# Performance work log

Hardware: AMD Instinct MI355X
Metric: run time of the kernel (lower is better)

The kernel has to match this reference:

```python
import jax, jax.numpy as jnp
import numpy as np

H, EXP, N, CONV = 1024, 2, 16, 4
INNER = H * EXP          # 2048
DTR = max(H // 16, 1)    # 64
BATCH, SEQ = 2, 1024


def setup_inputs() -> dict:
    key = jax.random.key(0)
    ks = jax.random.split(key, 16)
    g = lambda k, shape, s=0.02: (jax.random.normal(k, shape, dtype=jnp.float32) * s)
    return {
        "x": jax.random.normal(ks[0], (BATCH, SEQ, H), dtype=jnp.float32),
        "norm_w": jnp.ones((H,), jnp.float32),
        "norm_b": jnp.zeros((H,), jnp.float32),
        "in_w": g(ks[1], (H, 2 * INNER)),
        "in_b": jnp.zeros((2 * INNER,), jnp.float32),
        "conv_w": g(ks[2], (INNER, CONV), 0.1),   # depthwise kernel (torch weight[:,0,:])
        "conv_b": jnp.zeros((INNER,), jnp.float32),
        "bc_w": g(ks[3], (INNER, 2 * N)),
        "bc_b": jnp.zeros((2 * N,), jnp.float32),
        "dtr_w": g(ks[4], (INNER, DTR)),
        "dtr_b": jnp.zeros((DTR,), jnp.float32),
        "dt_w": g(ks[5], (DTR, INNER)),
        "dt_b": jnp.zeros((INNER,), jnp.float32),
        "out_w": g(ks[6], (INNER, H)),
        "out_b": jnp.zeros((H,), jnp.float32),
    }


def _forward(x, norm_w, norm_b, in_w, in_b, conv_w, conv_b,
             bc_w, bc_b, dtr_w, dtr_b, dt_w, dt_b, out_w, out_b):
    B, L, _ = x.shape
    # LayerNorm
    mu = x.mean(-1, keepdims=True)
    var = ((x - mu) ** 2).mean(-1, keepdims=True)
    normed = (x - mu) * jax.lax.rsqrt(var + 1e-5) * norm_w + norm_b
    # in_proj -> split x/z branches
    xz = normed @ in_w + in_b
    xb, z = xz[..., :INNER], xz[..., INNER:]
    # causal depthwise conv (torch pads both sides conv-1 then truncates to L == left-pad only)
    xp = jnp.pad(xb, ((0, 0), (CONV - 1, 0), (0, 0)))
    xc = sum(xp[:, k:k + L, :] * conv_w[:, k] for k in range(CONV)) + conv_b
    xa = jax.nn.silu(xc)                                  # [B,L,INNER]
    # B, C, dt projections
    bc = xa @ bc_w + bc_b
    Bm, Cm = bc[..., :N], bc[..., N:]                     # each [B,L,N]
    dt = jax.nn.softplus((xa @ dtr_w + dtr_b) @ dt_w + dt_b)
    dt = jnp.clip(dt, 0.001, 0.1)                         # [B,L,INNER]
    # discretize
    a_diag = -(jnp.arange(N, dtype=jnp.float32) + 1.0)
    a_bar = jnp.exp(dt[..., None] * a_diag)               # [B,L,INNER,N]
    dt_mean = dt.mean(axis=2, keepdims=True)[..., None]   # [B,L,1,1]
    bx = dt_mean * Bm[:, :, None, :] * xa[..., None]      # [B,L,INNER,N]
    # selective scan over time (h = a_t*h + bx_t; y_t = <C_t, h_t>)
    def step(h, ts):
        a_t, bx_t, c_t = ts
        h = a_t * h + bx_t
        y = jnp.einsum('bdn,bn->bd', h, c_t)
        return h, y
    h0 = jnp.zeros((B, INNER, N), x.dtype)
    _, ys = jax.lax.scan(step, h0, (a_bar.transpose(1, 0, 2, 3),
                                    bx.transpose(1, 0, 2, 3),
                                    Cm.transpose(1, 0, 2)))
    ssm_out = ys.transpose(1, 0, 2)                       # [B,L,INNER]
    gated = ssm_out * jax.nn.silu(z)
    return gated @ out_w + out_b


def reference(x, norm_w, norm_b, in_w, in_b, conv_w, conv_b,
              bc_w, bc_b, dtr_w, dtr_b, dt_w, dt_b, out_w, out_b):
    return _forward(x, norm_w, norm_b, in_w, in_b, conv_w, conv_b,
                    bc_w, bc_b, dtr_w, dtr_b, dt_w, dt_b, out_w, out_b)
```

## Files before the change

kernel.cpp:

```cpp
#include <hip/hip_runtime.h>
#include <math.h>

#define H      1024
#define INNER  2048
#define NST    16
#define SEQ    1024
#define ROWS   2048
#define XZW    (2*INNER)

typedef unsigned short u16;
typedef short bf16x8 __attribute__((ext_vector_type(8)));
typedef float f32x4 __attribute__((ext_vector_type(4)));

__device__ __forceinline__ u16 f2bf(float f) {
  unsigned u = __float_as_uint(f);
  return (u16)((u + 0x7FFF + ((u >> 16) & 1)) >> 16);
}
__device__ __forceinline__ float bf2f(u16 s) {
  return __uint_as_float(((unsigned)s) << 16);
}
__device__ __forceinline__ void gload16(const u16* g, u16* l) {
  __builtin_amdgcn_global_load_lds(
      (const __attribute__((address_space(1))) void*)g,
      (__attribute__((address_space(3))) void*)l, 16, 0, 0);
}

__global__ __launch_bounds__(256) void ln_kernel(
    const float* __restrict__ x, const float* __restrict__ w,
    const float* __restrict__ b, u16* __restrict__ ahi, u16* __restrict__ alo) {
  int row = blockIdx.x;
  int tid = threadIdx.x;
  const float4* xr = reinterpret_cast<const float4*>(x + (size_t)row * H);
  float4 v = xr[tid];
  float s = v.x + v.y + v.z + v.w;
  for (int o = 32; o > 0; o >>= 1) s += __shfl_down(s, o);
  __shared__ float r1[4], r2[4];
  int wv = tid >> 6;
  if ((tid & 63) == 0) r1[wv] = s;
  __syncthreads();
  float mu = (r1[0] + r1[1] + r1[2] + r1[3]) * (1.0f / H);
  float4 d;
  d.x = v.x - mu; d.y = v.y - mu; d.z = v.z - mu; d.w = v.w - mu;
  float sq = d.x*d.x + d.y*d.y + d.z*d.z + d.w*d.w;
  for (int o = 32; o > 0; o >>= 1) sq += __shfl_down(sq, o);
  if ((tid & 63) == 0) r2[wv] = sq;
  __syncthreads();
  float var = (r2[0] + r2[1] + r2[2] + r2[3]) * (1.0f / H);
  float rs = 1.0f / sqrtf(var + 1e-5f);
  float4 w4 = reinterpret_cast<const float4*>(w)[tid];
  float4 b4 = reinterpret_cast<const float4*>(b)[tid];
  float o0 = d.x * rs * w4.x + b4.x;
  float o1 = d.y * rs * w4.y + b4.y;
  float o2 = d.z * rs * w4.z + b4.z;
  float o3 = d.w * rs * w4.w + b4.w;
  ushort4 hh, ll;
  hh.x = f2bf(o0); ll.x = f2bf(o0 - bf2f(hh.x));
  hh.y = f2bf(o1); ll.y = f2bf(o1 - bf2f(hh.y));
  hh.z = f2bf(o2); ll.z = f2bf(o2 - bf2f(hh.z));
  hh.w = f2bf(o3); ll.w = f2bf(o3 - bf2f(hh.w));
  reinterpret_cast<ushort4*>(ahi + (size_t)row * H)[tid] = hh;
  reinterpret_cast<ushort4*>(alo + (size_t)row * H)[tid] = ll;
}

__global__ __launch_bounds__(256) void cvt_t_kernel(
    const float* __restrict__ W, u16* __restrict__ Thi, u16* __restrict__ Tlo,
    int K, int N) {
  __shared__ float t[32][33];
  int tx = threadIdx.x & 31, ty = threadIdx.x >> 5;
  int k0 = blockIdx.y * 32, n0 = blockIdx.x * 32;
#pragma unroll
  for (int r = 0; r < 4; ++r)
    t[ty + r * 8][tx] = W[(size_t)(k0 + ty + r * 8) * N + n0 + tx];
  __syncthreads();
#pragma unroll
  for (int r = 0; r < 4; ++r) {
    int row = ty + r * 8;
    float v = t[tx][row];
    u16 h = f2bf(v);
    size_t idx = (size_t)(n0 + row) * K + k0 + tx;
    Thi[idx] = h;
    Tlo[idx] = f2bf(v - bf2f(h));
  }
}

template <int BN_, bool ATOMIC>
__global__ __launch_bounds__(256) void gemm_mfma(
    const u16* __restrict__ a_hi, const u16* __restrict__ a_lo,
    const u16* __restrict__ b_hi, const u16* __restrict__ b_lo,
    const float* __restrict__ bias, float* __restrict__ C, int N,
    int Kstride, int Ksub) {
  constexpr int MN = BN_ / 32;
  constexpr int NB = BN_ / 16;
  constexpr int T  = 16 + 2 * NB;
  constexpr int CH = T / 4;
  constexpr int HALF = 128 * 32 * 2 + BN_ * 32 * 2;
  __shared__ __align__(16) u16 lds[2 * HALF];
  const int tid = threadIdx.x;
  const int lane = tid & 63;
  const int w = tid >> 6;
  const int m0 = blockIdx.y * 128;
  const int n0 = blockIdx.x * BN_;
  const int koff = blockIdx.z * Ksub;
  const int wr = (w >> 1) * 64;
  const int wc = (w & 1) * (BN_ / 2);
  const int s = lane >> 4;
  const int rl = lane & 15;
  f32x4 acc[4][MN];
#pragma unroll
  for (int m = 0; m < 4; ++m)
#pragma unroll
    for (int n = 0; n < MN; ++n)
#pragma unroll
      for (int r = 0; r < 4; ++r) acc[m][n][r] = 0.0f;

  auto stageF = [&](int buf, int k0) {
    u16* lbase = lds + buf * HALF;
    for (int c = w; c < T; c += 4) {
      const u16* gb; int cc, rg, lo;
      if (c < 8)            { gb = a_hi; cc = c;           rg = m0; lo = 0; }
      else if (c < 16)      { gb = a_lo; cc = c - 8;       rg = m0; lo = 128 * 32; }
      else if (c < 16 + NB) { gb = b_hi; cc = c - 16;      rg = n0; lo = 128 * 64; }
      else                  { gb = b_lo; cc = c - 16 - NB; rg = n0; lo = 128 * 64 + BN_ * 32; }
      int o = cc * 1024 + lane * 16;
      int row = o >> 6;
      int k8 = ((o >> 4) & 3) ^ ((row >> 1) & 3);
      gload16(gb + (size_t)(rg + row) * Kstride + k0 + k8 * 8,
              lbase + lo + cc * 512);
    }
  };

  const int NT = Ksub / 32;
  stageF(0, koff);
  asm volatile("s_waitcnt vmcnt(0)\n\ts_barrier" ::: "memory");
  int cur = 0;
  for (int t = 0; t < NT; ++t) {
    if (t + 1 < NT) {
      stageF(cur ^ 1, koff + (t + 1) * 32);
      if constexpr (CH == 8)
        asm volatile("s_waitcnt vmcnt(8)\n\ts_barrier" ::: "memory");
      else if constexpr (CH == 7)
        asm volatile("s_waitcnt vmcnt(7)\n\ts_barrier" ::: "memory");
      else
        asm volatile("s_waitcnt vmcnt(6)\n\ts_barrier" ::: "memory");
    } else {
      asm volatile("s_waitcnt vmcnt(0)\n\ts_barrier" ::: "memory");
    }
    const u16* lah = lds + cur * HALF;
    const u16* lal = lah + 128 * 32;
    const u16* lbh = lah + 128 * 64;
    const u16* lbl = lbh + BN_ * 32;
    bf16x8 ah[4], al[4], bh[MN], bl[MN];
#pragma unroll
    for (int m = 0; m < 4; ++m) {
      int r = wr + m * 16 + rl;
      int sw = (s ^ ((r >> 1) & 3)) * 8;
      ah[m] = *reinterpret_cast<const bf16x8*>(lah + r * 32 + sw);
      al[m] = *reinterpret_cast<const bf16x8*>(lal + r * 32 + sw);
    }
#pragma unroll
    for (int n = 0; n < MN; ++n) {
      int r = wc + n * 16 + rl;
      int sw = (s ^ ((r >> 1) & 3)) * 8;
      bh[n] = *reinterpret_cast<const bf16x8*>(lbh + r * 32 + sw);
      bl[n] = *reinterpret_cast<const bf16x8*>(lbl + r * 32 + sw);
    }
#pragma unroll
    for (int m = 0; m < 4; ++m)
#pragma unroll
      for (int n = 0; n < MN; ++n) {
        acc[m][n] = __builtin_amdgcn_mfma_f32_16x16x32_bf16(ah[m], bh[n], acc[m][n], 0, 0, 0);
        acc[m][n] = __builtin_amdgcn_mfma_f32_16x16x32_bf16(al[m], bh[n], acc[m][n], 0, 0, 0);
        acc[m][n] = __builtin_amdgcn_mfma_f32_16x16x32_bf16(ah[m], bl[n], acc[m][n], 0, 0, 0);
      }
    asm volatile("s_barrier" ::: "memory");
    cur ^= 1;
  }
#pragma unroll
  for (int n = 0; n < MN; ++n) {
    int col = n0 + wc + n * 16 + rl;
    float bv = ATOMIC ? 0.0f : bias[col];
#pragma unroll
    for (int m = 0; m < 4; ++m) {
      int r0 = m0 + wr + m * 16 + s * 4;
#pragma unroll
      for (int r = 0; r < 4; ++r) {
        if (ATOMIC)
          atomicAdd(&C[(size_t)(r0 + r) * N + col], acc[m][n][r]);
        else
          C[(size_t)(r0 + r) * N + col] = acc[m][n][r] + bv;
      }
    }
  }
}

__global__ __launch_bounds__(256) void conv_kernel(
    const float* __restrict__ xz, const float* __restrict__ cw,
    const float* __restrict__ cb, float* __restrict__ xa,
    u16* __restrict__ xahi, u16* __restrict__ xalo) {
  int row = blockIdx.x;
  int t = row & (SEQ - 1);
  int tid = threadIdx.x;
  for (int d = tid; d < INNER; d += 256) {
    float4 w = reinterpret_cast<const float4*>(cw)[d];
    float wj[4] = {w.x, w.y, w.z, w.w};
    float acc = cb[d];
#pragma unroll
    for (int j = 0; j < 4; ++j) {
      int ts = t - 3 + j;
      if (ts >= 0) acc = fmaf(xz[(size_t)(row - 3 + j) * XZW + d], wj[j], acc);
    }
    float sv = acc / (1.0f + __expf(-acc));
    size_t idx = (size_t)row * INNER + d;
    xa[idx] = sv;
    u16 hh = f2bf(sv);
    xahi[idx] = hh;
    xalo[idx] = f2bf(sv - bf2f(hh));
  }
}

__global__ __launch_bounds__(256) void bcd_init_kernel(
    const float* __restrict__ bc_b, const float* __restrict__ dtr_b,
    float* __restrict__ bcd) {
  int i = blockIdx.x * 256 + threadIdx.x;
  int col = i % 96;
  bcd[i] = (col < 32) ? bc_b[col] : dtr_b[col - 32];
}

__global__ __launch_bounds__(256) void out_init_kernel(
    const float* __restrict__ out_b, float* __restrict__ out) {
  int i = blockIdx.x * 256 + threadIdx.x;
  out[i] = out_b[i & (H - 1)];
}

__global__ __launch_bounds__(256) void dtsp_kernel(
    const float* __restrict__ bcd, const float* __restrict__ dt_w,
    const float* __restrict__ dt_b, float* __restrict__ dt,
    float* __restrict__ dtm, float* __restrict__ scanBC) {
  int tid = threadIdx.x;
  int row0 = blockIdx.x * 8;
  __shared__ float rl[8][64];
  __shared__ float psum[8][4];
  __shared__ float dtmrow[8];
  for (int i = tid; i < 512; i += 256)
    rl[i >> 6][i & 63] = bcd[(size_t)(row0 + (i >> 6)) * 96 + 32 + (i & 63)];
  __syncthreads();
  float lsum[8] = {};
  for (int j = 0; j < 8; ++j) {
    int d = tid + j * 256;
    float acc[8];
    float bb = dt_b[d];
#pragma unroll
    for (int r = 0; r < 8; ++r) acc[r] = bb;
#pragma unroll 8
    for (int k = 0; k < 64; ++k) {
      float w = dt_w[(size_t)k * INNER + d];
#pragma unroll
      for (int r = 0; r < 8; ++r) acc[r] = fmaf(rl[r][k], w, acc[r]);
    }
#pragma unroll
    for (int r = 0; r < 8; ++r) {
      float xv = acc[r];
      float sp = (xv > 15.0f) ? xv : log1pf(__expf(xv));
      float dv = fminf(fmaxf(sp, 1e-3f), 0.1f);
      dt[(size_t)(row0 + r) * INNER + d] = dv;
      lsum[r] += dv;
    }
  }
#pragma unroll
  for (int r = 0; r < 8; ++r) {
    float s = lsum[r];
    for (int o = 32; o > 0; o >>= 1) s += __shfl_down(s, o);
    if ((tid & 63) == 0) psum[r][tid >> 6] = s;
  }
  __syncthreads();
  if (tid < 8) {
    float v =
        (psum[tid][0] + psum[tid][1] + psum[tid][2] + psum[tid][3]) * (1.0f / INNER);
    dtm[row0 + tid] = v;
    dtmrow[tid] = v;
  }
  __syncthreads();
  int rr = tid >> 5, cc = tid & 31;
  float v = bcd[(size_t)(row0 + rr) * 96 + cc];
  if (cc < 16) v *= dtmrow[rr];
  scanBC[(size_t)(row0 + rr) * 32 + cc] = v;
}

__global__ __launch_bounds__(256) void scan1_kernel(
    const float* __restrict__ dt, const float* __restrict__ xa,
    const float* __restrict__ scanBC, float* __restrict__ Abuf,
    float* __restrict__ hbuf, int NC, int CL) {
  int tid = threadIdx.x;
  int dl = tid & 63;
  int NCB = NC >> 2;
  int bi = blockIdx.x;
  int cg = bi % NCB;
  int dg = (bi / NCB) & 31;
  int b = bi / (NCB * 32);
  int d = dg * 64 + dl;
  int c = cg * 4 + (tid >> 6);
  size_t r = (size_t)b * SEQ + (size_t)c * CL;
  const float* dtp = dt + r * INNER + d;
  const float* xap = xa + r * INNER + d;
  const float* bcp = scanBC + r * 32;
  float h[16];
#pragma unroll
  for (int n = 0; n < 16; ++n) h[n] = 0.0f;
  float S = 0.0f;
#pragma unroll 2
  for (int t = 0; t < CL; ++t) {
    float dtv = dtp[0];
    float xav = xap[0];
    float bB[16];
#pragma unroll
    for (int q = 0; q < 4; ++q)
      *reinterpret_cast<float4*>(&bB[q * 4]) =
          *reinterpret_cast<const float4*>(bcp + q * 4);
    S += dtv;
    float e1 = __expf(-dtv);
    float w = e1;
#pragma unroll
    for (int n = 0; n < 16; ++n) {
      h[n] = fmaf(w, h[n], xav * bB[n]);
      w *= e1;
    }
    dtp += INNER;
    xap += INNER;
    bcp += 32;
  }
  size_t base = (((size_t)b * NC + c) * INNER + d) * 16;
  float eS = __expf(-S);
  float A[16];
  float w = eS;
#pragma unroll
  for (int n = 0; n < 16; ++n) { A[n] = w; w *= eS; }
#pragma unroll
  for (int q = 0; q < 4; ++q) {
    *reinterpret_cast<float4*>(Abuf + base + q * 4) =
        *reinterpret_cast<float4*>(&A[q * 4]);
    *reinterpret_cast<float4*>(hbuf + base + q * 4) =
        *reinterpret_cast<float4*>(&h[q * 4]);
  }
}

__global__ __launch_bounds__(256) void scan2_kernel(
    const float* __restrict__ Abuf, float* __restrict__ hbuf, int NC) {
  int idx = blockIdx.x * 256 + threadIdx.x;
  size_t stride = (size_t)INNER * 16;
  size_t base = (size_t)(idx >> 15) * NC * stride + (size_t)(idx & 32767);
  float h = 0.0f;
  for (int c = 0; c < NC; ++c) {
    float A = Abuf[base];
    float hl = hbuf[base];
    hbuf[base] = h;
    h = fmaf(A, h, hl);
    base += stride;
  }
}

__global__ __launch_bounds__(256) void scan3_kernel(
    const float* __restrict__ dt, const float* __restrict__ xa,
    const float* __restrict__ scanBC, const float* __restrict__ xz,
    const float* __restrict__ hbuf, u16* __restrict__ ghi, u16* __restrict__ glo,
    int NC, int CL) {
  int tid = threadIdx.x;
  int dl = tid & 63;
  int NCB = NC >> 2;
  int bi = blockIdx.x;
  int cg = bi % NCB;
  int dg = (bi / NCB) & 31;
  int b = bi / (NCB * 32);
  int d = dg * 64 + dl;
  int c = cg * 4 + (tid >> 6);
  size_t r = (size_t)b * SEQ + (size_t)c * CL;
  const float* dtp = dt + r * INNER + d;
  const float* xap = xa + r * INNER + d;
  const float* bcp = scanBC + r * 32;
  const float* zp = xz + r * XZW + INNER + d;
  u16* ghp = ghi + r * INNER + d;
  u16* glp = glo + r * INNER + d;
  size_t hb = (((size_t)b * NC + c) * INNER + d) * 16;
  float h[16];
#pragma unroll
  for (int q = 0; q < 4; ++q)
    *reinterpret_cast<float4*>(&h[q * 4]) =
        *reinterpret_cast<const float4*>(hbuf + hb + q * 4);
#pragma unroll 2
  for (int t = 0; t < CL; ++t) {
    float dtv = dtp[0];
    float xav = xap[0];
    float zv = zp[0];
    float bB[16], cC[16];
#pragma unroll
    for (int q = 0; q < 4; ++q) {
      *reinterpret_cast<float4*>(&bB[q * 4]) =
          *reinterpret_cast<const float4*>(bcp + q * 4);
      *reinterpret_cast<float4*>(&cC[q * 4]) =
          *reinterpret_cast<const float4*>(bcp + 16 + q * 4);
    }
    float e1 = __expf(-dtv);
    float w = e1;
    float y = 0.0f;
#pragma unroll
    for (int n = 0; n < 16; ++n) {
      h[n] = fmaf(w, h[n], xav * bB[n]);
      w *= e1;
      y = fmaf(h[n], cC[n], y);
    }
    float sz = zv / (1.0f + __expf(-zv));
    float g = y * sz;
    u16 gh = f2bf(g);
    ghp[0] = gh;
    glp[0] = f2bf(g - bf2f(gh));
    dtp += INNER;
    xap += INNER;
    bcp += 32;
    zp += XZW;
    ghp += INNER;
    glp += INNER;
  }
}

extern "C" void kernel_launch(void* const* d_in, const int* in_sizes, int n_in,
                              void* d_out, int out_size, void* d_ws, size_t ws_size,
                              hipStream_t stream) {
  const float* x      = (const float*)d_in[0];
  const float* norm_w = (const float*)d_in[1];
  const float* norm_b = (const float*)d_in[2];
  const float* in_w   = (const float*)d_in[3];
  const float* in_b   = (const float*)d_in[4];
  const float* conv_w = (const float*)d_in[5];
  const float* conv_b = (const float*)d_in[6];
  const float* bc_w   = (const float*)d_in[7];
  const float* bc_b   = (const float*)d_in[8];
  const float* dtr_w  = (const float*)d_in[9];
  const float* dtr_b  = (const float*)d_in[10];
  const float* dt_w   = (const float*)d_in[11];
  const float* dt_b   = (const float*)d_in[12];
  const float* out_w  = (const float*)d_in[13];
  const float* out_b  = (const float*)d_in[14];

  float* ws = (float*)d_ws;
  float* xz     = ws;
  float* xa     = ws + 8388608;
  float* bcd    = ws + 12582912;
  float* dt     = ws + 12779520;
  float* dtm    = ws + 16973824;
  float* scanBC = ws + 16975872;
  u16* a1hi   = (u16*)(ws + 17041408);
  u16* a1lo   = (u16*)(ws + 18089984);
  u16* b1thi  = (u16*)(ws + 19138560);
  u16* b1tlo  = (u16*)(ws + 21235712);
  u16* xahi   = (u16*)(ws + 17041408);
  u16* xalo   = (u16*)(ws + 19138560);
  u16* bcdThi = (u16*)(ws + 21235712);
  u16* bcdTlo = (u16*)(ws + 21334016);
  u16* g3hi   = (u16*)(ws + 17041408);
  u16* g3lo   = (u16*)(ws + 19138560);
  u16* b3thi  = (u16*)(ws + 21235712);
  u16* b3tlo  = (u16*)(ws + 22284288);
  float* Abuf = ws + 23332864;
  const int NC = 64, CL = SEQ / NC;
  float* hbuf = Abuf + (size_t)NC * 65536;

  ln_kernel<<<ROWS, 256, 0, stream>>>(x, norm_w, norm_b, a1hi, a1lo);
  cvt_t_kernel<<<dim3(XZW / 32, H / 32), 256, 0, stream>>>(in_w, b1thi, b1tlo, H, XZW);
  gemm_mfma<128, false><<<dim3(XZW / 128, ROWS / 128, 1), 256, 0, stream>>>(
      a1hi, a1lo, b1thi, b1tlo, in_b, xz, XZW, H, H);
  conv_kernel<<<ROWS, 256, 0, stream>>>(xz, conv_w, conv_b, xa, xahi, xalo);
  cvt_t_kernel<<<dim3(1, INNER / 32), 256, 0, stream>>>(bc_w, bcdThi, bcdTlo,
                                                        INNER, 32);
  cvt_t_kernel<<<dim3(2, INNER / 32), 256, 0, stream>>>(
      dtr_w, bcdThi + 32 * 2048, bcdTlo + 32 * 2048, INNER, 64);
  bcd_init_kernel<<<ROWS * 96 / 256, 256, 0, stream>>>(bc_b, dtr_b, bcd);
  gemm_mfma<96, true><<<dim3(1, ROWS / 128, 16), 256, 0, stream>>>(
      xahi, xalo, bcdThi, bcdTlo, bc_b, bcd, 96, INNER, INNER / 16);
  dtsp_kernel<<<ROWS / 8, 256, 0, stream>>>(bcd, dt_w, dt_b, dt, dtm, scanBC);
  cvt_t_kernel<<<dim3(H / 32, INNER / 32), 256, 0, stream>>>(out_w, b3thi, b3tlo,
                                                             INNER, H);
  scan1_kernel<<<2 * 32 * (NC / 4), 256, 0, stream>>>(dt, xa, scanBC, Abuf, hbuf,
                                                      NC, CL);
  scan2_kernel<<<256, 256, 0, stream>>>(Abuf, hbuf, NC);
  scan3_kernel<<<2 * 32 * (NC / 4), 256, 0, stream>>>(dt, xa, scanBC, xz, hbuf,
                                                      g3hi, g3lo, NC, CL);
  out_init_kernel<<<ROWS * H / 256, 256, 0, stream>>>(out_b, (float*)d_out);
  gemm_mfma<64, true><<<dim3(H / 64, ROWS / 128, 2), 256, 0, stream>>>(
      g3hi, g3lo, b3thi, b3tlo, out_b, (float*)d_out, H, INNER, INNER / 2);
}
```

Before: 392.9 us.

## Replace atomic split-K accumulation with partial buffers and reduction kernels

The split-K GEMMs now write per-slice partial results into scratch buffers instead of doing fp32 atomicAdd into a pre-initialized output. Separate reduction kernels then sum the slices and add the bias. The output projection goes from 2 to 4 K-splits. This removes atomic contention and the init kernels, and the result becomes deterministic. The cost is extra scratch traffic, one more pass over memory, and reuse of the xz and Abuf buffers as scratch space.

```diff
diff --git a/kernel.cpp b/kernel.cpp
--- a/kernel.cpp
+++ b/kernel.cpp
@@ -83,12 +83,12 @@
   }
 }
 
-template <int BN_, bool ATOMIC>
+template <int BN_, int MODE>
 __global__ __launch_bounds__(256) void gemm_mfma(
     const u16* __restrict__ a_hi, const u16* __restrict__ a_lo,
     const u16* __restrict__ b_hi, const u16* __restrict__ b_lo,
     const float* __restrict__ bias, float* __restrict__ C, int N,
-    int Kstride, int Ksub) {
+    int Kstride, int Ksub, int Mtot) {
   constexpr int MN = BN_ / 32;
   constexpr int NB = BN_ / 16;
   constexpr int T  = 16 + 2 * NB;
@@ -175,22 +175,47 @@
     asm volatile("s_barrier" ::: "memory");
     cur ^= 1;
   }
+  float* Cz = (MODE == 1) ? C + (size_t)blockIdx.z * Mtot * N : C;
 #pragma unroll
   for (int n = 0; n < MN; ++n) {
     int col = n0 + wc + n * 16 + rl;
-    float bv = ATOMIC ? 0.0f : bias[col];
+    float bv = (MODE == 0) ? bias[col] : 0.0f;
 #pragma unroll
     for (int m = 0; m < 4; ++m) {
       int r0 = m0 + wr + m * 16 + s * 4;
 #pragma unroll
-      for (int r = 0; r < 4; ++r) {
-        if (ATOMIC)
-          atomicAdd(&C[(size_t)(r0 + r) * N + col], acc[m][n][r]);
-        else
-          C[(size_t)(r0 + r) * N + col] = acc[m][n][r] + bv;
-      }
-    }
-  }
+      for (int r = 0; r < 4; ++r)
+        Cz[(size_t)(r0 + r) * N + col] = acc[m][n][r] + bv;
+    }
+  }
+}
+
+__global__ __launch_bounds__(256) void red3_kernel(
+    const float* __restrict__ p, const float* __restrict__ out_b,
+    float* __restrict__ out) {
+  int i = (blockIdx.x * 256 + threadIdx.x) * 4;
+  float4 a = *reinterpret_cast<const float4*>(p + i);
+  float4 b = *reinterpret_cast<const float4*>(p + 2097152 + i);
+  float4 c = *reinterpret_cast<const float4*>(p + 2 * 2097152 + i);
+  float4 d = *reinterpret_cast<const float4*>(p + 3 * 2097152 + i);
+  float4 bb = *reinterpret_cast<const float4*>(out_b + (i & (H - 1)));
+  float4 o;
+  o.x = a.x + b.x + c.x + d.x + bb.x;
+  o.y = a.y + b.y + c.y + d.y + bb.y;
+  o.z = a.z + b.z + c.z + d.z + bb.z;
+  o.w = a.w + b.w + c.w + d.w + bb.w;
+  *reinterpret_cast<float4*>(out + i) = o;
+}
+
+__global__ __launch_bounds__(256) void redb_kernel(
+    const float* __restrict__ p, const float* __restrict__ bc_b,
+    const float* __restrict__ dtr_b, float* __restrict__ bcd) {
+  int i = blockIdx.x * 256 + threadIdx.x;
+  int col = i % 96;
+  float s = (col < 32) ? bc_b[col] : dtr_b[col - 32];
+#pragma unroll
+  for (int k = 0; k < 16; ++k) s += p[(size_t)k * (ROWS * 96) + i];
+  bcd[i] = s;
 }
 
 __global__ __launch_bounds__(256) void conv_kernel(
@@ -216,20 +241,6 @@
     xahi[idx] = hh;
     xalo[idx] = f2bf(sv - bf2f(hh));
   }
-}
-
-__global__ __launch_bounds__(256) void bcd_init_kernel(
-    const float* __restrict__ bc_b, const float* __restrict__ dtr_b,
-    float* __restrict__ bcd) {
-  int i = blockIdx.x * 256 + threadIdx.x;
-  int col = i % 96;
-  bcd[i] = (col < 32) ? bc_b[col] : dtr_b[col - 32];
-}
-
-__global__ __launch_bounds__(256) void out_init_kernel(
-    const float* __restrict__ out_b, float* __restrict__ out) {
-  int i = blockIdx.x * 256 + threadIdx.x;
-  out[i] = out_b[i & (H - 1)];
 }
 
 __global__ __launch_bounds__(256) void dtsp_kernel(
@@ -462,19 +473,21 @@
   float* Abuf = ws + 23332864;
   const int NC = 64, CL = SEQ / NC;
   float* hbuf = Abuf + (size_t)NC * 65536;
+  float* partb = Abuf;
+  float* part3 = xz;
 
   ln_kernel<<<ROWS, 256, 0, stream>>>(x, norm_w, norm_b, a1hi, a1lo);
   cvt_t_kernel<<<dim3(XZW / 32, H / 32), 256, 0, stream>>>(in_w, b1thi, b1tlo, H, XZW);
-  gemm_mfma<128, false><<<dim3(XZW / 128, ROWS / 128, 1), 256, 0, stream>>>(
-      a1hi, a1lo, b1thi, b1tlo, in_b, xz, XZW, H, H);
+  gemm_mfma<128, 0><<<dim3(XZW / 128, ROWS / 128, 1), 256, 0, stream>>>(
+      a1hi, a1lo, b1thi, b1tlo, in_b, xz, XZW, H, H, ROWS);
   conv_kernel<<<ROWS, 256, 0, stream>>>(xz, conv_w, conv_b, xa, xahi, xalo);
   cvt_t_kernel<<<dim3(1, INNER / 32), 256, 0, stream>>>(bc_w, bcdThi, bcdTlo,
                                                         INNER, 32);
   cvt_t_kernel<<<dim3(2, INNER / 32), 256, 0, stream>>>(
       dtr_w, bcdThi + 32 * 2048, bcdTlo + 32 * 2048, INNER, 64);
-  bcd_init_kernel<<<ROWS * 96 / 256, 256, 0, stream>>>(bc_b, dtr_b, bcd);
-  gemm_mfma<96, true><<<dim3(1, ROWS / 128, 16), 256, 0, stream>>>(
-      xahi, xalo, bcdThi, bcdTlo, bc_b, bcd, 96, INNER, INNER / 16);
+  gemm_mfma<96, 1><<<dim3(1, ROWS / 128, 16), 256, 0, stream>>>(
+      xahi, xalo, bcdThi, bcdTlo, nullptr, partb, 96, INNER, INNER / 16, ROWS);
+  redb_kernel<<<ROWS * 96 / 256, 256, 0, stream>>>(partb, bc_b, dtr_b, bcd);
   dtsp_kernel<<<ROWS / 8, 256, 0, stream>>>(bcd, dt_w, dt_b, dt, dtm, scanBC);
   cvt_t_kernel<<<dim3(H / 32, INNER / 32), 256, 0, stream>>>(out_w, b3thi, b3tlo,
                                                              INNER, H);
@@ -483,7 +496,7 @@
   scan2_kernel<<<256, 256, 0, stream>>>(Abuf, hbuf, NC);
   scan3_kernel<<<2 * 32 * (NC / 4), 256, 0, stream>>>(dt, xa, scanBC, xz, hbuf,
                                                       g3hi, g3lo, NC, CL);
-  out_init_kernel<<<ROWS * H / 256, 256, 0, stream>>>(out_b, (float*)d_out);
-  gemm_mfma<64, true><<<dim3(H / 64, ROWS / 128, 2), 256, 0, stream>>>(
-      g3hi, g3lo, b3thi, b3tlo, out_b, (float*)d_out, H, INNER, INNER / 2);
-}
+  gemm_mfma<64, 1><<<dim3(H / 64, ROWS / 128, 4), 256, 0, stream>>>(
+      g3hi, g3lo, b3thi, b3tlo, nullptr, part3, H, INNER, INNER / 4, ROWS);
+  red3_kernel<<<ROWS * H / 1024, 256, 0, stream>>>(part3, out_b, (float*)d_out);
+}
```

Result: no change. 400.6 us (+2.0%).
